# Kernel optimization log

Measured on AMD Instinct MI355X. Metric: run time of the kernel, lower is better.

Reference implementation:

```python
import jax, jax.numpy as jnp
import numpy as np

N_EMBED = 2048
NUM_EXPERTS = 64
TOP_K = 8
B, S = 4, 8192


def setup_inputs() -> dict:
    key = jax.random.key(0)
    ks = jax.random.split(key, 8)
    scale = 1.0 / np.sqrt(N_EMBED)
    return {
        "x": jax.random.normal(ks[0], (B, S, N_EMBED), dtype=jnp.float32),
        "eps": jax.random.normal(ks[1], (B, S, NUM_EXPERTS), dtype=jnp.float32),
        "w_router": jax.random.uniform(ks[2], (N_EMBED, NUM_EXPERTS), jnp.float32, -scale, scale),
        "b_router": jax.random.uniform(ks[3], (NUM_EXPERTS,), jnp.float32, -scale, scale),
        "w_noise": jax.random.uniform(ks[4], (N_EMBED, NUM_EXPERTS), jnp.float32, -scale, scale),
        "b_noise": jax.random.uniform(ks[5], (NUM_EXPERTS,), jnp.float32, -scale, scale),
        "w_skip": jax.random.uniform(ks[6], (N_EMBED, 1), jnp.float32, -scale, scale),
        "b_skip": jax.random.uniform(ks[7], (1,), jnp.float32, -scale, scale),
    }


def reference(x, eps, w_router, b_router, w_noise, b_noise, w_skip, b_skip):
    # Router and noise logits: [B, S, E]
    logits = jnp.einsum("bsd,de->bse", x, w_router) + b_router
    noise_logits = jnp.einsum("bsd,de->bse", x, w_noise) + b_noise
    # noisy_logits = logits + randn * softplus(noise_logits); randn passed as eps
    noisy_logits = logits + eps * jax.nn.softplus(noise_logits)
    # top-k + scatter(-inf) + softmax == softmax over top-k values scattered back
    top_vals, indices = jax.lax.top_k(noisy_logits, TOP_K)  # [B,S,K]
    gates = jax.nn.softmax(top_vals, axis=-1)  # [B,S,K]
    onehot = jax.nn.one_hot(indices, NUM_EXPERTS, dtype=x.dtype)  # [B,S,K,E]
    router_output = jnp.einsum("bsk,bske->bse", gates, onehot)  # zeros off top-k
    # Sigmoid skip gate: [B, S, 1]
    skip_prob = jax.nn.sigmoid(jnp.einsum("bsd,do->bso", x, w_skip) + b_skip)
    return router_output, indices, skip_prob
```

## Files before the change

kernel.cpp:

```cpp
#include <hip/hip_runtime.h>
#include <math.h>

#define NTOK   32768
#define D      2048
#define E      64
#define TOPK   8

#define BLOCK  256
#define TM     64
#define BK     32
#define NCHUNK (D / BK)
#define NBLK   (NTOK / TM)

#define WBF_BYTES (NCHUNK * 16384)

#define BUF_STRIDE 24576
#define WSK_OFF 49152
#define SP_OFF  57344
#define SMEM_BYTES 57600
#define LG_STR 133

#define TIE_EPS 2e-4f

typedef __bf16 bf16x8 __attribute__((ext_vector_type(8)));
typedef float  f32x4  __attribute__((ext_vector_type(4)));

#define AS1 __attribute__((address_space(1)))
#define AS3 __attribute__((address_space(3)))

__device__ __forceinline__ unsigned short f2bf_rne(float f) {
    unsigned int u = __float_as_uint(f);
    u += 0x7FFFu + ((u >> 16) & 1u);
    return (unsigned short)(u >> 16);
}

__device__ __forceinline__ void split_pack8(const float* xv, uint4& hv, uint4& lv) {
    unsigned int h[8], l[8];
#pragma unroll
    for (int j = 0; j < 8; ++j) {
        unsigned short hb = f2bf_rne(xv[j]);
        float hf = __uint_as_float(((unsigned int)hb) << 16);
        unsigned short lb = f2bf_rne(xv[j] - hf);
        h[j] = hb; l[j] = lb;
    }
    hv.x = h[0] | (h[1] << 16); hv.y = h[2] | (h[3] << 16);
    hv.z = h[4] | (h[5] << 16); hv.w = h[6] | (h[7] << 16);
    lv.x = l[0] | (l[1] << 16); lv.y = l[2] | (l[3] << 16);
    lv.z = l[4] | (l[5] << 16); lv.w = l[6] | (l[7] << 16);
}

__global__ __launch_bounds__(256) void convert_w_kernel(
    const float* __restrict__ wr, const float* __restrict__ wn, char* __restrict__ wbf)
{
    int u = blockIdx.x * 256 + threadIdx.x;
    int col  = u & 127;
    int koct = (u >> 7) & 3;
    int c    = u >> 9;
    const float* src = (col < 64)
        ? (wr + (size_t)(c * BK + koct * 8) * E + col)
        : (wn + (size_t)(c * BK + koct * 8) * E + (col - 64));
    float xv[8];
#pragma unroll
    for (int j = 0; j < 8; ++j) xv[j] = src[(size_t)j * E];
    uint4 hv, lv;
    split_pack8(xv, hv, lv);
    char* dst = wbf + (size_t)c * 16384 + (size_t)(koct * 128 + col) * 16;
    *(uint4*)dst = hv;
    *(uint4*)(dst + 8192) = lv;
}

__global__ __launch_bounds__(BLOCK, 2) void router_kernel(
    const float* __restrict__ x, const float* __restrict__ eps,
    const char* __restrict__ wbf,
    const float* __restrict__ b_router, const float* __restrict__ b_noise,
    const float* __restrict__ w_skip, const float* __restrict__ b_skip,
    float* __restrict__ out_router, float* __restrict__ out_idx,
    float* __restrict__ out_skip, int* __restrict__ flags, int cap)
{
    __shared__ __attribute__((aligned(16))) char smem[SMEM_BYTES];
    const int tid = threadIdx.x;
    const int tokBase = blockIdx.x * TM;

    const int lane = tid & 63;
    const int wv   = __builtin_amdgcn_readfirstlane(tid >> 6);
    const int q    = lane >> 4;
    const int m    = lane & 15;

    const int tokA  = tid >> 2;
    const int koctA = tid & 3;
    const int fragA = (koctA << 6) + (tokA ^ (koctA << 2));
    const float* xptr = x + (size_t)(tokBase + tokA) * D + koctA * 8;

    f32x4 acc[4][2];
#pragma unroll
    for (int tt = 0; tt < 4; ++tt)
#pragma unroll
        for (int cw = 0; cw < 2; ++cw) acc[tt][cw] = (f32x4){0.f, 0.f, 0.f, 0.f};
    float skipAcc = 0.f;

    float* wsk = (float*)(smem + WSK_OFF);

    auto issueB = [&](int c, int buf) {
        const char* src = wbf + (size_t)c * 16384;
        char* dstbase = smem + buf * BUF_STRIDE + 8192;
#pragma unroll
        for (int r = 0; r < 4; ++r) {
            int seg = r * 4 + wv;
            __builtin_amdgcn_global_load_lds(
                (const AS1 unsigned int*)(src + seg * 1024 + lane * 16),
                (AS3 unsigned int*)(dstbase + seg * 1024), 16, 0, 0);
        }
    };

    auto storeA = [&](int buf, float4 a0, float4 a1) {
        float xv[8] = {a0.x, a0.y, a0.z, a0.w, a1.x, a1.y, a1.z, a1.w};
        uint4 hv, lv;
        split_pack8(xv, hv, lv);
        char* ab = smem + buf * BUF_STRIDE;
        *(uint4*)(ab + fragA * 16) = hv;
        *(uint4*)(ab + 4096 + fragA * 16) = lv;
    };

    auto skipFma = [&](float4 a0, float4 a1, int c) {
        const float* wk = wsk + c * BK + koctA * 8;
        skipAcc = fmaf(a0.x, wk[0], skipAcc); skipAcc = fmaf(a0.y, wk[1], skipAcc);
        skipAcc = fmaf(a0.z, wk[2], skipAcc); skipAcc = fmaf(a0.w, wk[3], skipAcc);
        skipAcc = fmaf(a1.x, wk[4], skipAcc); skipAcc = fmaf(a1.y, wk[5], skipAcc);
        skipAcc = fmaf(a1.z, wk[6], skipAcc); skipAcc = fmaf(a1.w, wk[7], skipAcc);
    };

    auto compute = [&](int buf) {
        const char* ab = smem + buf * BUF_STRIDE;
        const char* bb = ab + 8192;
        uint4 ah[4], al[4], bh[2], bl[2];
#pragma unroll
        for (int tt = 0; tt < 4; ++tt) {
            int f = (q << 6) + (((tt << 4) + m) ^ (q << 2));
            ah[tt] = *(const uint4*)(ab + f * 16);
            al[tt] = *(const uint4*)(ab + 4096 + f * 16);
        }
#pragma unroll
        for (int cw = 0; cw < 2; ++cw) {
            int f = (q << 7) + (wv << 5) + (cw << 4) + m;
            bh[cw] = *(const uint4*)(bb + f * 16);
            bl[cw] = *(const uint4*)(bb + 8192 + f * 16);
        }
#pragma unroll
        for (int tt = 0; tt < 4; ++tt)
#pragma unroll
            for (int cw = 0; cw < 2; ++cw) {
                bf16x8 Ah = __builtin_bit_cast(bf16x8, ah[tt]);
                bf16x8 Al = __builtin_bit_cast(bf16x8, al[tt]);
                bf16x8 Bh = __builtin_bit_cast(bf16x8, bh[cw]);
                bf16x8 Bl = __builtin_bit_cast(bf16x8, bl[cw]);
                acc[tt][cw] = __builtin_amdgcn_mfma_f32_16x16x32_bf16(Ah, Bh, acc[tt][cw], 0, 0, 0);
                acc[tt][cw] = __builtin_amdgcn_mfma_f32_16x16x32_bf16(Ah, Bl, acc[tt][cw], 0, 0, 0);
                acc[tt][cw] = __builtin_amdgcn_mfma_f32_16x16x32_bf16(Al, Bh, acc[tt][cw], 0, 0, 0);
            }
    };

#pragma unroll
    for (int r = 0; r < 2; ++r) {
        int i4 = tid + 256 * r;
        ((float4*)wsk)[i4] = ((const float4*)w_skip)[i4];
    }
    float4 ra0 = *(const float4*)(xptr);
    float4 ra1 = *(const float4*)(xptr + 4);
    issueB(0, 0);
    storeA(0, ra0, ra1);
    __syncthreads();
    skipFma(ra0, ra1, 0);

    for (int c = 0; c < NCHUNK; ++c) {
        int cur = c & 1;
        float4 rb0, rb1;
        if (c + 1 < NCHUNK) {
            rb0 = *(const float4*)(xptr + (c + 1) * BK);
            rb1 = *(const float4*)(xptr + (c + 1) * BK + 4);
            issueB(c + 1, cur ^ 1);
        }
        compute(cur);
        if (c + 1 < NCHUNK) {
            storeA(cur ^ 1, rb0, rb1);
            skipFma(rb0, rb1, c + 1);
        }
        __syncthreads();
    }

    float* lg = (float*)smem;
#pragma unroll
    for (int tt = 0; tt < 4; ++tt)
#pragma unroll
        for (int cw = 0; cw < 2; ++cw) {
#pragma unroll
            for (int reg = 0; reg < 4; ++reg) {
                int token = tt * 16 + q * 4 + reg;
                int col = wv * 32 + cw * 16 + m;
                lg[token * LG_STR + col] = acc[tt][cw][reg];
            }
        }

    skipAcc += __shfl_xor(skipAcc, 1);
    skipAcc += __shfl_xor(skipAcc, 2);
    if ((tid & 3) == 0) ((float*)(smem + SP_OFF))[tokA] = skipAcc;
    __syncthreads();

    if (tid < 64) {
        const int t = tid;
        const int tok = tokBase + t;
        float* row = lg + t * LG_STR;

        float sv = ((float*)(smem + SP_OFF))[t] + b_skip[0];
        out_skip[tok] = 1.f / (1.f + expf(-sv));

        const float4* epsr = (const float4*)(eps + (size_t)tok * E);
#pragma unroll 4
        for (int e4 = 0; e4 < 16; ++e4) {
            float4 ep = epsr[e4];
            float epv[4] = {ep.x, ep.y, ep.z, ep.w};
#pragma unroll
            for (int u2 = 0; u2 < 4; ++u2) {
                int e = e4 * 4 + u2;
                float lgv = row[e] + b_router[e];
                float nl  = row[64 + e] + b_noise[e];
                float sp  = fmaxf(nl, 0.f) + log1pf(expf(-fabsf(nl)));
                row[e] = lgv + epv[u2] * sp;
            }
        }

        float vals[9];
        int idxs[8];
        for (int p = 0; p < 9; ++p) {
            float best = -INFINITY;
            int bi = 0;
            for (int e = 0; e < 64; ++e) {
                float v = row[e];
                if (v > best) { best = v; bi = e; }
            }
            vals[p] = best;
            if (p < 8) idxs[p] = bi;
            row[bi] = -INFINITY;
        }

        float mg = 1e30f;
#pragma unroll
        for (int p = 0; p < 8; ++p) mg = fminf(mg, vals[p] - vals[p + 1]);
        if (mg < TIE_EPS) {
            int slot = atomicAdd(flags, 1);
            if (slot < cap) flags[2 + slot] = tok;
        }

        float mx = vals[0];
        float g[8], s = 0.f;
#pragma unroll
        for (int p = 0; p < 8; ++p) { g[p] = expf(vals[p] - mx); s += g[p]; }
        float inv = 1.f / s;

        float* rrow = row + 64;
#pragma unroll
        for (int e = 0; e < 64; ++e) rrow[e] = 0.f;
#pragma unroll
        for (int p = 0; p < 8; ++p) rrow[idxs[p]] = g[p] * inv;
#pragma unroll
        for (int e4 = 0; e4 < 16; ++e4) {
            float4 o = make_float4(rrow[e4 * 4], rrow[e4 * 4 + 1],
                                   rrow[e4 * 4 + 2], rrow[e4 * 4 + 3]);
            *(float4*)(out_router + (size_t)tok * E + e4 * 4) = o;
        }
        float4 i0 = make_float4((float)idxs[0], (float)idxs[1], (float)idxs[2], (float)idxs[3]);
        float4 i1 = make_float4((float)idxs[4], (float)idxs[5], (float)idxs[6], (float)idxs[7]);
        *(float4*)(out_idx + (size_t)tok * TOPK)     = i0;
        *(float4*)(out_idx + (size_t)tok * TOPK + 4) = i1;
    }
}

__global__ __launch_bounds__(256) void fixup_kernel(
    const float* __restrict__ x, const float* __restrict__ eps,
    const float* __restrict__ w_router, const float* __restrict__ b_router,
    const float* __restrict__ w_noise, const float* __restrict__ b_noise,
    float* __restrict__ out_router, float* __restrict__ out_idx,
    const int* __restrict__ flags, int cap)
{
    __shared__ double smR[4][64];
    __shared__ double smN[4][64];
    __shared__ double noisy[64];
    const int tid  = threadIdx.x;
    const int lane = tid & 63;
    const int qw   = tid >> 6;

    int count = flags[0];
    if (count > cap) count = cap;

    for (int i = blockIdx.x; i < count; i += gridDim.x) {
        int tok = flags[2 + i];
        const float4* xr4 = (const float4*)(x + (size_t)tok * D + qw * 512);
        const float* wrB = w_router + (size_t)(qw * 512) * E + lane;
        const float* wnB = w_noise  + (size_t)(qw * 512) * E + lane;

        double pr0 = 0, pr1 = 0, pr2 = 0, pr3 = 0;
        double pn0 = 0, pn1 = 0, pn2 = 0, pn3 = 0;
        for (int it = 0; it < 128; ++it) {
            float4 xv = xr4[it];
            const float* wr = wrB + (size_t)(it * 4) * E;
            const float* wn = wnB + (size_t)(it * 4) * E;
            pr0 += (double)xv.x * (double)wr[0];
            pr1 += (double)xv.y * (double)wr[E];
            pr2 += (double)xv.z * (double)wr[2 * E];
            pr3 += (double)xv.w * (double)wr[3 * E];
            pn0 += (double)xv.x * (double)wn[0];
            pn1 += (double)xv.y * (double)wn[E];
            pn2 += (double)xv.z * (double)wn[2 * E];
            pn3 += (double)xv.w * (double)wn[3 * E];
        }
        smR[qw][lane] = (pr0 + pr1) + (pr2 + pr3);
        smN[qw][lane] = (pn0 + pn1) + (pn2 + pn3);
        __syncthreads();

        if (tid < 64) {
            double lgv = smR[0][tid] + smR[1][tid] + smR[2][tid] + smR[3][tid] + (double)b_router[tid];
            double nl  = smN[0][tid] + smN[1][tid] + smN[2][tid] + smN[3][tid] + (double)b_noise[tid];
            double sp  = fmax(nl, 0.0) + log1p(exp(-fabs(nl)));
            noisy[tid] = lgv + (double)eps[(size_t)tok * E + tid] * sp;
        }
        __syncthreads();

        if (tid == 0) {
            double tmp[64];
            for (int j = 0; j < 64; ++j) tmp[j] = noisy[j];
            double vals[8]; int idxs[8];
            for (int p = 0; p < 8; ++p) {
                double best = -1e300; int bi = 0;
                for (int j = 0; j < 64; ++j)
                    if (tmp[j] > best) { best = tmp[j]; bi = j; }
                vals[p] = best; idxs[p] = bi; tmp[bi] = -1e300;
            }
            double mx = vals[0], s = 0.0, g[8];
            for (int p = 0; p < 8; ++p) { g[p] = exp(vals[p] - mx); s += g[p]; }
            float rowv[64];
            for (int j = 0; j < 64; ++j) rowv[j] = 0.f;
            for (int p = 0; p < 8; ++p) rowv[idxs[p]] = (float)(g[p] / s);
            for (int j = 0; j < 64; ++j) out_router[(size_t)tok * E + j] = rowv[j];
            for (int p = 0; p < 8; ++p) out_idx[(size_t)tok * TOPK + p] = (float)idxs[p];
        }
        __syncthreads();
    }
}

extern "C" void kernel_launch(void* const* d_in, const int* in_sizes, int n_in,
                              void* d_out, int out_size, void* d_ws, size_t ws_size,
                              hipStream_t stream) {
    const float* x        = (const float*)d_in[0];
    const float* eps      = (const float*)d_in[1];
    const float* w_router = (const float*)d_in[2];
    const float* b_router = (const float*)d_in[3];
    const float* w_noise  = (const float*)d_in[4];
    const float* b_noise  = (const float*)d_in[5];
    const float* w_skip   = (const float*)d_in[6];
    const float* b_skip   = (const float*)d_in[7];

    float* out = (float*)d_out;
    float* out_router = out;
    float* out_idx    = out + (size_t)NTOK * E;
    float* out_skip   = out_idx + (size_t)NTOK * TOPK;

    char* wbf  = (char*)d_ws;
    int* flags = (int*)((char*)d_ws + WBF_BYTES);
    int cap = 0;
    if (ws_size > WBF_BYTES + 16) {
        size_t c = (ws_size - WBF_BYTES - 8) / 4;
        cap = (c > 16384) ? 16384 : (int)c;
    }

    hipMemsetAsync((char*)d_ws + WBF_BYTES, 0, 8, stream);

    convert_w_kernel<<<dim3(128), dim3(256), 0, stream>>>(w_router, w_noise, wbf);

    router_kernel<<<dim3(NBLK), dim3(BLOCK), 0, stream>>>(
        x, eps, wbf, b_router, b_noise, w_skip, b_skip,
        out_router, out_idx, out_skip, flags, cap);

    fixup_kernel<<<dim3(512), dim3(256), 0, stream>>>(
        x, eps, w_router, b_router, w_noise, b_noise,
        out_router, out_idx, flags, cap);
}
```

Baseline: 543.5 us.

## Load GEMM operands directly to registers, dropping LDS staging and barriers

The main K loop stops staging A (x split into bf16 hi/lo) and B (pre-split weights) through double-buffered LDS with per-chunk __syncthreads. Each wave now loads its own MFMA fragments straight from global memory into registers, using a two-generation register ping-pong for prefetch. Waves are remapped to 2 token groups × 2 column halves, and the skip-gate dot product reads w_skip from global memory. This removes LDS traffic and barriers and cuts LDS use, but every wave pair now redundantly loads and splits the same x rows and weight fragments, and register pressure rises.

```diff
diff --git a/kernel.cpp b/kernel.cpp
--- a/kernel.cpp
+++ b/kernel.cpp
@@ -14,19 +14,14 @@
 
 #define WBF_BYTES (NCHUNK * 16384)
 
-#define BUF_STRIDE 24576
-#define WSK_OFF 49152
-#define SP_OFF  57344
-#define SMEM_BYTES 57600
 #define LG_STR 133
+#define SP_OFF  34048
+#define SMEM_BYTES 34304
 
 #define TIE_EPS 2e-4f
 
 typedef __bf16 bf16x8 __attribute__((ext_vector_type(8)));
 typedef float  f32x4  __attribute__((ext_vector_type(4)));
-
-#define AS1 __attribute__((address_space(1)))
-#define AS3 __attribute__((address_space(3)))
 
 __device__ __forceinline__ unsigned short f2bf_rne(float f) {
     unsigned int u = __float_as_uint(f);
@@ -83,126 +78,104 @@
 
     const int lane = tid & 63;
     const int wv   = __builtin_amdgcn_readfirstlane(tid >> 6);
+    const int tg   = wv >> 1;
+    const int ch   = wv & 1;
     const int q    = lane >> 4;
     const int m    = lane & 15;
 
-    const int tokA  = tid >> 2;
-    const int koctA = tid & 3;
-    const int fragA = (koctA << 6) + (tokA ^ (koctA << 2));
-    const float* xptr = x + (size_t)(tokBase + tokA) * D + koctA * 8;
-
-    f32x4 acc[4][2];
-#pragma unroll
-    for (int tt = 0; tt < 4; ++tt)
-#pragma unroll
-        for (int cw = 0; cw < 2; ++cw) acc[tt][cw] = (f32x4){0.f, 0.f, 0.f, 0.f};
-    float skipAcc = 0.f;
-
-    float* wsk = (float*)(smem + WSK_OFF);
-
-    auto issueB = [&](int c, int buf) {
-        const char* src = wbf + (size_t)c * 16384;
-        char* dstbase = smem + buf * BUF_STRIDE + 8192;
-#pragma unroll
-        for (int r = 0; r < 4; ++r) {
-            int seg = r * 4 + wv;
-            __builtin_amdgcn_global_load_lds(
-                (const AS1 unsigned int*)(src + seg * 1024 + lane * 16),
-                (AS3 unsigned int*)(dstbase + seg * 1024), 16, 0, 0);
-        }
+    const float* xlane = x + (size_t)(tokBase + tg * 32 + m) * D + q * 8;
+    const char*  blane = wbf + (size_t)((q << 7) + (ch << 6) + m) * 16;
+    const float* wklane = w_skip + q * 8;
+
+    f32x4 acc[2][4];
+#pragma unroll
+    for (int tt = 0; tt < 2; ++tt)
+#pragma unroll
+        for (int cw = 0; cw < 4; ++cw) acc[tt][cw] = (f32x4){0.f, 0.f, 0.f, 0.f};
+    float skipAcc[2] = {0.f, 0.f};
+
+    struct Gen {
+        float4 a[2][2];
+        uint4  b[4][2];
+        float4 wk[2];
     };
 
-    auto storeA = [&](int buf, float4 a0, float4 a1) {
-        float xv[8] = {a0.x, a0.y, a0.z, a0.w, a1.x, a1.y, a1.z, a1.w};
-        uint4 hv, lv;
-        split_pack8(xv, hv, lv);
-        char* ab = smem + buf * BUF_STRIDE;
-        *(uint4*)(ab + fragA * 16) = hv;
-        *(uint4*)(ab + 4096 + fragA * 16) = lv;
+    auto loadGen = [&](Gen& g, int c) {
+        const float* xp = xlane + c * BK;
+#pragma unroll
+        for (int tt = 0; tt < 2; ++tt) {
+            g.a[tt][0] = *(const float4*)(xp + (size_t)tt * 16 * D);
+            g.a[tt][1] = *(const float4*)(xp + (size_t)tt * 16 * D + 4);
+        }
+        const char* bp = blane + (size_t)c * 16384;
+#pragma unroll
+        for (int cw = 0; cw < 4; ++cw) {
+            g.b[cw][0] = *(const uint4*)(bp + cw * 256);
+            g.b[cw][1] = *(const uint4*)(bp + cw * 256 + 8192);
+        }
+        g.wk[0] = *(const float4*)(wklane + c * BK);
+        g.wk[1] = *(const float4*)(wklane + c * BK + 4);
     };
 
-    auto skipFma = [&](float4 a0, float4 a1, int c) {
-        const float* wk = wsk + c * BK + koctA * 8;
-        skipAcc = fmaf(a0.x, wk[0], skipAcc); skipAcc = fmaf(a0.y, wk[1], skipAcc);
-        skipAcc = fmaf(a0.z, wk[2], skipAcc); skipAcc = fmaf(a0.w, wk[3], skipAcc);
-        skipAcc = fmaf(a1.x, wk[4], skipAcc); skipAcc = fmaf(a1.y, wk[5], skipAcc);
-        skipAcc = fmaf(a1.z, wk[6], skipAcc); skipAcc = fmaf(a1.w, wk[7], skipAcc);
-    };
-
-    auto compute = [&](int buf) {
-        const char* ab = smem + buf * BUF_STRIDE;
-        const char* bb = ab + 8192;
-        uint4 ah[4], al[4], bh[2], bl[2];
-#pragma unroll
-        for (int tt = 0; tt < 4; ++tt) {
-            int f = (q << 6) + (((tt << 4) + m) ^ (q << 2));
-            ah[tt] = *(const uint4*)(ab + f * 16);
-            al[tt] = *(const uint4*)(ab + 4096 + f * 16);
-        }
-#pragma unroll
-        for (int cw = 0; cw < 2; ++cw) {
-            int f = (q << 7) + (wv << 5) + (cw << 4) + m;
-            bh[cw] = *(const uint4*)(bb + f * 16);
-            bl[cw] = *(const uint4*)(bb + 8192 + f * 16);
-        }
-#pragma unroll
-        for (int tt = 0; tt < 4; ++tt)
-#pragma unroll
-            for (int cw = 0; cw < 2; ++cw) {
-                bf16x8 Ah = __builtin_bit_cast(bf16x8, ah[tt]);
-                bf16x8 Al = __builtin_bit_cast(bf16x8, al[tt]);
-                bf16x8 Bh = __builtin_bit_cast(bf16x8, bh[cw]);
-                bf16x8 Bl = __builtin_bit_cast(bf16x8, bl[cw]);
+    auto computeGen = [&](Gen& g) {
+#pragma unroll
+        for (int tt = 0; tt < 2; ++tt) {
+            float xv[8] = {g.a[tt][0].x, g.a[tt][0].y, g.a[tt][0].z, g.a[tt][0].w,
+                           g.a[tt][1].x, g.a[tt][1].y, g.a[tt][1].z, g.a[tt][1].w};
+            uint4 hv, lv;
+            split_pack8(xv, hv, lv);
+            bf16x8 Ah = __builtin_bit_cast(bf16x8, hv);
+            bf16x8 Al = __builtin_bit_cast(bf16x8, lv);
+#pragma unroll
+            for (int cw = 0; cw < 4; ++cw) {
+                bf16x8 Bh = __builtin_bit_cast(bf16x8, g.b[cw][0]);
+                bf16x8 Bl = __builtin_bit_cast(bf16x8, g.b[cw][1]);
                 acc[tt][cw] = __builtin_amdgcn_mfma_f32_16x16x32_bf16(Ah, Bh, acc[tt][cw], 0, 0, 0);
                 acc[tt][cw] = __builtin_amdgcn_mfma_f32_16x16x32_bf16(Ah, Bl, acc[tt][cw], 0, 0, 0);
                 acc[tt][cw] = __builtin_amdgcn_mfma_f32_16x16x32_bf16(Al, Bh, acc[tt][cw], 0, 0, 0);
             }
+            float s = skipAcc[tt];
+            s = fmaf(xv[0], g.wk[0].x, s); s = fmaf(xv[1], g.wk[0].y, s);
+            s = fmaf(xv[2], g.wk[0].z, s); s = fmaf(xv[3], g.wk[0].w, s);
+            s = fmaf(xv[4], g.wk[1].x, s); s = fmaf(xv[5], g.wk[1].y, s);
+            s = fmaf(xv[6], g.wk[1].z, s); s = fmaf(xv[7], g.wk[1].w, s);
+            skipAcc[tt] = s;
+        }
     };
 
-#pragma unroll
-    for (int r = 0; r < 2; ++r) {
-        int i4 = tid + 256 * r;
-        ((float4*)wsk)[i4] = ((const float4*)w_skip)[i4];
-    }
-    float4 ra0 = *(const float4*)(xptr);
-    float4 ra1 = *(const float4*)(xptr + 4);
-    issueB(0, 0);
-    storeA(0, ra0, ra1);
-    __syncthreads();
-    skipFma(ra0, ra1, 0);
-
-    for (int c = 0; c < NCHUNK; ++c) {
-        int cur = c & 1;
-        float4 rb0, rb1;
-        if (c + 1 < NCHUNK) {
-            rb0 = *(const float4*)(xptr + (c + 1) * BK);
-            rb1 = *(const float4*)(xptr + (c + 1) * BK + 4);
-            issueB(c + 1, cur ^ 1);
-        }
-        compute(cur);
-        if (c + 1 < NCHUNK) {
-            storeA(cur ^ 1, rb0, rb1);
-            skipFma(rb0, rb1, c + 1);
-        }
-        __syncthreads();
+    Gen gA, gB;
+    loadGen(gA, 0);
+#pragma unroll 1
+    for (int c = 0; c < NCHUNK; c += 2) {
+        loadGen(gB, c + 1);
+        computeGen(gA);
+        if (c + 2 < NCHUNK) loadGen(gA, c + 2);
+        computeGen(gB);
     }
 
     float* lg = (float*)smem;
 #pragma unroll
-    for (int tt = 0; tt < 4; ++tt)
-#pragma unroll
-        for (int cw = 0; cw < 2; ++cw) {
+    for (int tt = 0; tt < 2; ++tt)
+#pragma unroll
+        for (int cw = 0; cw < 4; ++cw) {
 #pragma unroll
             for (int reg = 0; reg < 4; ++reg) {
-                int token = tt * 16 + q * 4 + reg;
-                int col = wv * 32 + cw * 16 + m;
+                int token = tg * 32 + tt * 16 + q * 4 + reg;
+                int col = ch * 64 + cw * 16 + m;
                 lg[token * LG_STR + col] = acc[tt][cw][reg];
             }
         }
 
-    skipAcc += __shfl_xor(skipAcc, 1);
-    skipAcc += __shfl_xor(skipAcc, 2);
-    if ((tid & 3) == 0) ((float*)(smem + SP_OFF))[tokA] = skipAcc;
+#pragma unroll
+    for (int tt = 0; tt < 2; ++tt) {
+        skipAcc[tt] += __shfl_xor(skipAcc[tt], 16);
+        skipAcc[tt] += __shfl_xor(skipAcc[tt], 32);
+    }
+    if (ch == 0 && lane < 16) {
+        float* sp = (float*)(smem + SP_OFF);
+        sp[tg * 32 + lane]      = skipAcc[0];
+        sp[tg * 32 + 16 + lane] = skipAcc[1];
+    }
     __syncthreads();
 
     if (tid < 64) {
```

Result: no change. 549.9 us (+1.2%).

## Halve token tile, read bf16 weights from global, and widen K stage

Applied to the files above, without the earlier changes.

The router GEMM now uses 32-token tiles with 64-wide K stages. The bf16-split weight fragments are read directly from global memory (relying on cache) instead of being staged into LDS with global_load_lds. This shrinks LDS use and doubles the grid, which should raise occupancy and parallelism. The hi/lo split uses packed bf16 conversion, the tie epsilon for fixups is loosened, the fixup loop is unrolled, and the fixup grid is enlarged. The cost is more global and L2 traffic for weights and more fixup candidates from the wider tie threshold.

```diff
diff --git a/kernel.cpp b/kernel.cpp
--- a/kernel.cpp
+++ b/kernel.cpp
@@ -7,26 +7,27 @@
 #define TOPK   8
 
 #define BLOCK  256
-#define TM     64
-#define BK     32
-#define NCHUNK (D / BK)
-#define NBLK   (NTOK / TM)
-
-#define WBF_BYTES (NCHUNK * 16384)
-
-#define BUF_STRIDE 24576
-#define WSK_OFF 49152
-#define SP_OFF  57344
-#define SMEM_BYTES 57600
-#define LG_STR 133
-
-#define TIE_EPS 2e-4f
+#define TM2    32
+#define NBLK2  (NTOK / TM2)
+#define KS     64
+#define NS     (D / KS)
+
+#define WBF_BYTES (64 * 16384)
+
+#define FLAGS_OFF   WBF_BYTES
+
+#define A_HI(b)   ((b) * 8192)
+#define A_LO(b)   ((b) * 8192 + 4096)
+#define WSK2_OFF  16384
+#define SPS2_OFF  24576
+#define SMEM2     24704
+#define LG_STR    133
+
+#define TIE_EPS 3e-4f
 
 typedef __bf16 bf16x8 __attribute__((ext_vector_type(8)));
+typedef __bf16 bf16x2 __attribute__((ext_vector_type(2)));
 typedef float  f32x4  __attribute__((ext_vector_type(4)));
-
-#define AS1 __attribute__((address_space(1)))
-#define AS3 __attribute__((address_space(3)))
 
 __device__ __forceinline__ unsigned short f2bf_rne(float f) {
     unsigned int u = __float_as_uint(f);
@@ -47,6 +48,26 @@
     hv.z = h[4] | (h[5] << 16); hv.w = h[6] | (h[7] << 16);
     lv.x = l[0] | (l[1] << 16); lv.y = l[2] | (l[3] << 16);
     lv.z = l[4] | (l[5] << 16); lv.w = l[6] | (l[7] << 16);
+}
+
+__device__ __forceinline__ unsigned int pk2(float a, float b) {
+    bf16x2 p;
+    p[0] = (__bf16)a; p[1] = (__bf16)b;
+    return __builtin_bit_cast(unsigned int, p);
+}
+__device__ __forceinline__ void split_pack8_v2(const float* xv, uint4& hv, uint4& lv) {
+    unsigned int h[4], l[4];
+#pragma unroll
+    for (int p = 0; p < 4; ++p) {
+        float a = xv[2 * p], b = xv[2 * p + 1];
+        unsigned int hu = pk2(a, b);
+        float fa = __uint_as_float(hu << 16);
+        float fb = __uint_as_float(hu & 0xFFFF0000u);
+        h[p] = hu;
+        l[p] = pk2(a - fa, b - fb);
+    }
+    hv.x = h[0]; hv.y = h[1]; hv.z = h[2]; hv.w = h[3];
+    lv.x = l[0]; lv.y = l[1]; lv.z = l[2]; lv.w = l[3];
 }
 
 __global__ __launch_bounds__(256) void convert_w_kernel(
@@ -57,8 +78,8 @@
     int koct = (u >> 7) & 3;
     int c    = u >> 9;
     const float* src = (col < 64)
-        ? (wr + (size_t)(c * BK + koct * 8) * E + col)
-        : (wn + (size_t)(c * BK + koct * 8) * E + (col - 64));
+        ? (wr + (size_t)(c * 32 + koct * 8) * E + col)
+        : (wn + (size_t)(c * 32 + koct * 8) * E + (col - 64));
     float xv[8];
 #pragma unroll
     for (int j = 0; j < 8; ++j) xv[j] = src[(size_t)j * E];
@@ -69,148 +90,136 @@
     *(uint4*)(dst + 8192) = lv;
 }
 
-__global__ __launch_bounds__(BLOCK, 2) void router_kernel(
-    const float* __restrict__ x, const float* __restrict__ eps,
-    const char* __restrict__ wbf,
+__global__ __launch_bounds__(BLOCK) void router32_kernel(
+    const float* __restrict__ x, const char* __restrict__ wbf,
+    const float* __restrict__ w_skip, const float* __restrict__ eps,
     const float* __restrict__ b_router, const float* __restrict__ b_noise,
-    const float* __restrict__ w_skip, const float* __restrict__ b_skip,
+    const float* __restrict__ b_skip,
     float* __restrict__ out_router, float* __restrict__ out_idx,
     float* __restrict__ out_skip, int* __restrict__ flags, int cap)
 {
-    __shared__ __attribute__((aligned(16))) char smem[SMEM_BYTES];
+    __shared__ __attribute__((aligned(16))) char smem[SMEM2];
     const int tid = threadIdx.x;
-    const int tokBase = blockIdx.x * TM;
+    const int tokBase = blockIdx.x * TM2;
 
     const int lane = tid & 63;
     const int wv   = __builtin_amdgcn_readfirstlane(tid >> 6);
     const int q    = lane >> 4;
     const int m    = lane & 15;
 
-    const int tokA  = tid >> 2;
-    const int koctA = tid & 3;
-    const int fragA = (koctA << 6) + (tokA ^ (koctA << 2));
-    const float* xptr = x + (size_t)(tokBase + tokA) * D + koctA * 8;
-
-    f32x4 acc[4][2];
-#pragma unroll
-    for (int tt = 0; tt < 4; ++tt)
+    const int tokS = tid >> 3;
+    const int k8S  = tid & 7;
+    const float* xstage = x + (size_t)(tokBase + tokS) * D + k8S * 8;
+    float* wsk = (float*)(smem + WSK2_OFF);
+
+    const char* blane = wbf + (size_t)((q << 7) + (wv << 5) + m) * 16;
+
+    f32x4 acc[2][2];
+#pragma unroll
+    for (int tt = 0; tt < 2; ++tt)
 #pragma unroll
         for (int cw = 0; cw < 2; ++cw) acc[tt][cw] = (f32x4){0.f, 0.f, 0.f, 0.f};
     float skipAcc = 0.f;
-
-    float* wsk = (float*)(smem + WSK_OFF);
-
-    auto issueB = [&](int c, int buf) {
-        const char* src = wbf + (size_t)c * 16384;
-        char* dstbase = smem + buf * BUF_STRIDE + 8192;
-#pragma unroll
-        for (int r = 0; r < 4; ++r) {
-            int seg = r * 4 + wv;
-            __builtin_amdgcn_global_load_lds(
-                (const AS1 unsigned int*)(src + seg * 1024 + lane * 16),
-                (AS3 unsigned int*)(dstbase + seg * 1024), 16, 0, 0);
-        }
-    };
 
     auto storeA = [&](int buf, float4 a0, float4 a1) {
         float xv[8] = {a0.x, a0.y, a0.z, a0.w, a1.x, a1.y, a1.z, a1.w};
         uint4 hv, lv;
-        split_pack8(xv, hv, lv);
-        char* ab = smem + buf * BUF_STRIDE;
-        *(uint4*)(ab + fragA * 16) = hv;
-        *(uint4*)(ab + 4096 + fragA * 16) = lv;
+        split_pack8_v2(xv, hv, lv);
+        int slot = (k8S << 5) + (tokS ^ k8S);
+        *(uint4*)(smem + A_HI(buf) + slot * 16) = hv;
+        *(uint4*)(smem + A_LO(buf) + slot * 16) = lv;
     };
 
-    auto skipFma = [&](float4 a0, float4 a1, int c) {
-        const float* wk = wsk + c * BK + koctA * 8;
+    auto skipFma = [&](float4 a0, float4 a1, int s) {
+        const float* wk = wsk + s * KS + k8S * 8;
         skipAcc = fmaf(a0.x, wk[0], skipAcc); skipAcc = fmaf(a0.y, wk[1], skipAcc);
         skipAcc = fmaf(a0.z, wk[2], skipAcc); skipAcc = fmaf(a0.w, wk[3], skipAcc);
         skipAcc = fmaf(a1.x, wk[4], skipAcc); skipAcc = fmaf(a1.y, wk[5], skipAcc);
         skipAcc = fmaf(a1.z, wk[6], skipAcc); skipAcc = fmaf(a1.w, wk[7], skipAcc);
     };
 
-    auto compute = [&](int buf) {
-        const char* ab = smem + buf * BUF_STRIDE;
-        const char* bb = ab + 8192;
-        uint4 ah[4], al[4], bh[2], bl[2];
-#pragma unroll
-        for (int tt = 0; tt < 4; ++tt) {
-            int f = (q << 6) + (((tt << 4) + m) ^ (q << 2));
-            ah[tt] = *(const uint4*)(ab + f * 16);
-            al[tt] = *(const uint4*)(ab + 4096 + f * 16);
-        }
-#pragma unroll
-        for (int cw = 0; cw < 2; ++cw) {
-            int f = (q << 7) + (wv << 5) + (cw << 4) + m;
-            bh[cw] = *(const uint4*)(bb + f * 16);
-            bl[cw] = *(const uint4*)(bb + 8192 + f * 16);
-        }
-#pragma unroll
-        for (int tt = 0; tt < 4; ++tt)
+    auto compute = [&](int buf, int s) {
+#pragma unroll
+        for (int kk = 0; kk < 2; ++kk) {
+            const int K8 = kk * 4 + q;
+            uint4 ah[2], al[2], bh[2], bl[2];
+#pragma unroll
+            for (int tt = 0; tt < 2; ++tt) {
+                int slot = (K8 << 5) + ((tt * 16 + m) ^ K8);
+                ah[tt] = *(const uint4*)(smem + A_HI(buf) + slot * 16);
+                al[tt] = *(const uint4*)(smem + A_LO(buf) + slot * 16);
+            }
+            const char* bp = blane + (size_t)(2 * s + kk) * 16384;
 #pragma unroll
             for (int cw = 0; cw < 2; ++cw) {
+                bh[cw] = *(const uint4*)(bp + cw * 256);
+                bl[cw] = *(const uint4*)(bp + cw * 256 + 8192);
+            }
+#pragma unroll
+            for (int tt = 0; tt < 2; ++tt) {
                 bf16x8 Ah = __builtin_bit_cast(bf16x8, ah[tt]);
                 bf16x8 Al = __builtin_bit_cast(bf16x8, al[tt]);
-                bf16x8 Bh = __builtin_bit_cast(bf16x8, bh[cw]);
-                bf16x8 Bl = __builtin_bit_cast(bf16x8, bl[cw]);
-                acc[tt][cw] = __builtin_amdgcn_mfma_f32_16x16x32_bf16(Ah, Bh, acc[tt][cw], 0, 0, 0);
-                acc[tt][cw] = __builtin_amdgcn_mfma_f32_16x16x32_bf16(Ah, Bl, acc[tt][cw], 0, 0, 0);
-                acc[tt][cw] = __builtin_amdgcn_mfma_f32_16x16x32_bf16(Al, Bh, acc[tt][cw], 0, 0, 0);
-            }
+#pragma unroll
+                for (int cw = 0; cw < 2; ++cw) {
+                    bf16x8 Bh = __builtin_bit_cast(bf16x8, bh[cw]);
+                    bf16x8 Bl = __builtin_bit_cast(bf16x8, bl[cw]);
+                    acc[tt][cw] = __builtin_amdgcn_mfma_f32_16x16x32_bf16(Ah, Bh, acc[tt][cw], 0, 0, 0);
+                    acc[tt][cw] = __builtin_amdgcn_mfma_f32_16x16x32_bf16(Ah, Bl, acc[tt][cw], 0, 0, 0);
+                    acc[tt][cw] = __builtin_amdgcn_mfma_f32_16x16x32_bf16(Al, Bh, acc[tt][cw], 0, 0, 0);
+                }
+            }
+        }
     };
 
-#pragma unroll
-    for (int r = 0; r < 2; ++r) {
-        int i4 = tid + 256 * r;
-        ((float4*)wsk)[i4] = ((const float4*)w_skip)[i4];
-    }
-    float4 ra0 = *(const float4*)(xptr);
-    float4 ra1 = *(const float4*)(xptr + 4);
-    issueB(0, 0);
+    ((float4*)wsk)[tid]       = ((const float4*)w_skip)[tid];
+    ((float4*)wsk)[tid + 256] = ((const float4*)w_skip)[tid + 256];
+    float4 ra0 = *(const float4*)(xstage);
+    float4 ra1 = *(const float4*)(xstage + 4);
+    __syncthreads();
     storeA(0, ra0, ra1);
+    skipFma(ra0, ra1, 0);
     __syncthreads();
-    skipFma(ra0, ra1, 0);
-
-    for (int c = 0; c < NCHUNK; ++c) {
-        int cur = c & 1;
+
+#pragma unroll 1
+    for (int s = 0; s < NS; ++s) {
+        int cur = s & 1;
         float4 rb0, rb1;
-        if (c + 1 < NCHUNK) {
-            rb0 = *(const float4*)(xptr + (c + 1) * BK);
-            rb1 = *(const float4*)(xptr + (c + 1) * BK + 4);
-            issueB(c + 1, cur ^ 1);
-        }
-        compute(cur);
-        if (c + 1 < NCHUNK) {
+        if (s + 1 < NS) {
+            rb0 = *(const float4*)(xstage + (s + 1) * KS);
+            rb1 = *(const float4*)(xstage + (s + 1) * KS + 4);
+        }
+        compute(cur, s);
+        if (s + 1 < NS) {
             storeA(cur ^ 1, rb0, rb1);
-            skipFma(rb0, rb1, c + 1);
+            skipFma(rb0, rb1, s + 1);
         }
         __syncthreads();
     }
 
     float* lg = (float*)smem;
 #pragma unroll
-    for (int tt = 0; tt < 4; ++tt)
-#pragma unroll
-        for (int cw = 0; cw < 2; ++cw) {
+    for (int tt = 0; tt < 2; ++tt)
+#pragma unroll
+        for (int cw = 0; cw < 2; ++cw)
 #pragma unroll
             for (int reg = 0; reg < 4; ++reg) {
                 int token = tt * 16 + q * 4 + reg;
                 int col = wv * 32 + cw * 16 + m;
                 lg[token * LG_STR + col] = acc[tt][cw][reg];
             }
-        }
 
     skipAcc += __shfl_xor(skipAcc, 1);
     skipAcc += __shfl_xor(skipAcc, 2);
-    if ((tid & 3) == 0) ((float*)(smem + SP_OFF))[tokA] = skipAcc;
+    skipAcc += __shfl_xor(skipAcc, 4);
+    if (k8S == 0) ((float*)(smem + SPS2_OFF))[tokS] = skipAcc;
     __syncthreads();
 
-    if (tid < 64) {
+    if (tid < TM2) {
         const int t = tid;
         const int tok = tokBase + t;
         float* row = lg + t * LG_STR;
 
-        float sv = ((float*)(smem + SP_OFF))[t] + b_skip[0];
+        float sv = ((float*)(smem + SPS2_OFF))[t] + b_skip[0];
         out_skip[tok] = 1.f / (1.f + expf(-sv));
 
         const float4* epsr = (const float4*)(eps + (size_t)tok * E);
@@ -299,6 +308,7 @@
 
         double pr0 = 0, pr1 = 0, pr2 = 0, pr3 = 0;
         double pn0 = 0, pn1 = 0, pn2 = 0, pn3 = 0;
+#pragma unroll 4
         for (int it = 0; it < 128; ++it) {
             float4 xv = xr4[it];
             const float* wr = wrB + (size_t)(it * 4) * E;
@@ -364,22 +374,22 @@
     float* out_skip   = out_idx + (size_t)NTOK * TOPK;
 
     char* wbf  = (char*)d_ws;
-    int* flags = (int*)((char*)d_ws + WBF_BYTES);
+    int* flags = (int*)((char*)d_ws + FLAGS_OFF);
+
     int cap = 0;
-    if (ws_size > WBF_BYTES + 16) {
-        size_t c = (ws_size - WBF_BYTES - 8) / 4;
+    if (ws_size > FLAGS_OFF + 16) {
+        size_t c = (ws_size - FLAGS_OFF - 8) / 4;
         cap = (c > 16384) ? 16384 : (int)c;
     }
 
-    hipMemsetAsync((char*)d_ws + WBF_BYTES, 0, 8, stream);
-
     convert_w_kernel<<<dim3(128), dim3(256), 0, stream>>>(w_router, w_noise, wbf);
-
-    router_kernel<<<dim3(NBLK), dim3(BLOCK), 0, stream>>>(
-        x, eps, wbf, b_router, b_noise, w_skip, b_skip,
+    hipMemsetAsync((char*)d_ws + FLAGS_OFF, 0, 8, stream);
+
+    router32_kernel<<<dim3(NBLK2), dim3(BLOCK), 0, stream>>>(
+        x, wbf, w_skip, eps, b_router, b_noise, b_skip,
         out_router, out_idx, out_skip, flags, cap);
 
-    fixup_kernel<<<dim3(512), dim3(256), 0, stream>>>(
+    fixup_kernel<<<dim3(8192), dim3(256), 0, stream>>>(
         x, eps, w_router, b_router, w_noise, b_noise,
         out_router, out_idx, flags, cap);
 }
```

After: 544.4 us. No clear change (+0.2%).
